# Optimization experiments

Measured on AMD Instinct MI355X. Metric: run time of the kernel, lower is better.

The kernel has to match this reference:

```python
import jax, jax.numpy as jnp
import numpy as np

N_NODES = 100000


def gcn_conv(x, edge_index, W, b, n_nodes):
    """PyG GCNConv: out = D^-1/2 (A + I) D^-1/2 (x @ W^T) + b."""
    src, dst = edge_index[0], edge_index[1]
    loop = jnp.arange(n_nodes, dtype=src.dtype)
    src = jnp.concatenate([src, loop])  # [E + N]
    dst = jnp.concatenate([dst, loop])
    # degree of each node as aggregation target (includes self loop)
    deg = jax.ops.segment_sum(jnp.ones_like(src, dtype=x.dtype), dst,
                              num_segments=n_nodes)
    deg_inv_sqrt = jnp.where(deg > 0, jax.lax.rsqrt(deg), 0.0)
    norm = deg_inv_sqrt[src] * deg_inv_sqrt[dst]  # [E + N]
    h = x @ W.T  # [N, out_dim]  (transform BEFORE propagate, as in PyG)
    msg = h[src] * norm[:, None]  # gather + scale  [E + N, out_dim]
    out = jax.ops.segment_sum(msg, dst, num_segments=n_nodes)  # scatter-add
    return out + b


def setup_inputs() -> dict:
    key = jax.random.key(0)
    k_x, k_e, k_w1, k_b1, k_w2, k_b2 = jax.random.split(key, 6)
    in_dim, hidden = 128, 16
    n_edges = 3200000
    x = jax.random.normal(k_x, (N_NODES, in_dim), dtype=jnp.float32)
    edge_index = jax.random.randint(k_e, (2, n_edges), 0, N_NODES,
                                    dtype=jnp.int64)
    # Glorot-ish init for the linear weights (PyG Linear stores [out, in])
    W1 = jax.random.normal(k_w1, (hidden, in_dim), dtype=jnp.float32) / np.sqrt(in_dim)
    b1 = jnp.zeros((hidden,), dtype=jnp.float32)
    W2 = jax.random.normal(k_w2, (1, hidden), dtype=jnp.float32) / np.sqrt(hidden)
    b2 = jnp.zeros((1,), dtype=jnp.float32)
    return {"x": x, "edge_index": edge_index,
            "W1": W1, "b1": b1, "W2": W2, "b2": b2}


def reference(x, edge_index, W1, b1, W2, b2):
    n = x.shape[0]
    h = jax.nn.relu(gcn_conv(x, edge_index, W1, b1, n))  # [N, hidden]
    out = gcn_conv(h, edge_index, W2, b2, n)  # [N, 1]
    return out.squeeze(-1)  # [N]
```

## Files before the change

### kernel.cpp

```cpp
#include <hip/hip_runtime.h>

#define IN_DIM 128
#define HID 16
#define BSHIFT 8
#define BMASK  255
#define BCAP   9216
#define MID    4608
#define PCH    8192
#define FTHR   512
#define EPT    (PCH / FTHR)
#define TSCALE 4096.0f
#define ZSCALE 262144.0f

__global__ void init_kernel(const unsigned int* ei, int* flag, int* gcur) {
    int tid = blockIdx.x * blockDim.x + threadIdx.x;
    if (tid < 4096) gcur[tid] = 0;
    if (tid == 0) {
        int zeros = 0;
        for (int j = 0; j < 8; ++j)
            if (ei[2 * j + 1] == 0u) zeros++;
        *flag = (zeros >= 7) ? 1 : 0;
    }
}

__device__ __forceinline__ int edge_at(const void* ei, long long idx, int is64) {
    if (is64) return (int)((const long long*)ei)[idx];
    return ((const int*)ei)[idx];
}

__global__ __launch_bounds__(FTHR) void fat_kernel(const void* ei, long long E,
        int* gcur, unsigned int* __restrict__ binned, int NB, const int* flag,
        const float* __restrict__ x, const float* __restrict__ W1,
        short* __restrict__ ts16, int N, int pblk) {
    __shared__ float smem[4 * 128 * 17];
    int tid = threadIdx.x;
    if ((int)blockIdx.x < pblk) {
        int* cnt = (int*)smem;
        int* wbase = cnt + 1024;
        for (int i = tid; i < NB; i += FTHR) cnt[i] = 0;
        __syncthreads();
        const int is64 = *flag;
        const long long e0 = (long long)blockIdx.x * PCH;

        int sA[EPT], dA[EPT];
        if (e0 + PCH <= E) {
            if (is64) {
                const long long* p = (const long long*)ei;
#pragma unroll
                for (int j = 0; j < EPT; ++j) sA[j] = (int)p[e0 + j * FTHR + tid];
#pragma unroll
                for (int j = 0; j < EPT; ++j) dA[j] = (int)p[E + e0 + j * FTHR + tid];
            } else {
                const int* p = (const int*)ei;
#pragma unroll
                for (int j = 0; j < EPT; ++j) sA[j] = p[e0 + j * FTHR + tid];
#pragma unroll
                for (int j = 0; j < EPT; ++j) dA[j] = p[E + e0 + j * FTHR + tid];
            }
        } else {
#pragma unroll
            for (int j = 0; j < EPT; ++j) {
                long long e = e0 + j * FTHR + tid;
                bool ok = e < E;
                sA[j] = ok ? edge_at(ei, e, is64) : 0;
                dA[j] = ok ? edge_at(ei, E + e, is64) : -(BMASK + 1);
            }
        }

        unsigned int v[EPT];
        unsigned int br[EPT];
#pragma unroll
        for (int j = 0; j < EPT; ++j) {
            int b = dA[j] >> BSHIFT;
            bool ok = dA[j] >= 0;
            int r = ok ? atomicAdd(&cnt[b], 1) : 0;
            v[j]  = ((unsigned int)sA[j] << BSHIFT) | (unsigned int)(dA[j] & BMASK);
            br[j] = ok ? (((unsigned int)b << 16) | (unsigned int)r) : 0xFFFFFFFFu;
        }
        __syncthreads();
        const int q = (int)(blockIdx.x & 3);
        int* gc = gcur + q * 1024;
        for (int i = tid; i < NB; i += FTHR) {
            int c = cnt[i];
            wbase[i] = c ? atomicAdd(&gc[i], c) : 0;
        }
        __syncthreads();
        const int regBase = (q >> 1) * MID;
        const bool down = (q & 1);
#pragma unroll
        for (int j = 0; j < EPT; ++j) {
            if (br[j] != 0xFFFFFFFFu) {
                int b = (int)(br[j] >> 16);
                int r = (int)(br[j] & 0xFFFFu);
                int w = wbase[b] + r;
                if (w < MID) {
                    int pos = regBase + (down ? (MID - 1 - w) : w);
                    binned[(size_t)b * BCAP + pos] = v[j];
                }
            }
        }
    } else {
        const int nb = (int)blockIdx.x - pblk;
        const int lane = tid & 63;
        const int kq = __builtin_amdgcn_readfirstlane(tid >> 7);
        const int half = (tid >> 6) & 1;
        const int nl = half * 64 + lane;
        const int node = nb * 128 + nl;

        float acc[HID];
#pragma unroll
        for (int o = 0; o < HID; ++o) acc[o] = 0.f;
        if (node < N) {
            const float* xp = &x[(size_t)node * IN_DIM + kq * 32];
            float4 xv[8];
#pragma unroll
            for (int j = 0; j < 8; ++j) xv[j] = ((const float4*)xp)[j];
            const float* wp = &W1[kq * 32];
#pragma unroll
            for (int kk = 0; kk < 32; ++kk) {
                float xs = ((const float*)xv)[kk];
#pragma unroll
                for (int o = 0; o < HID; ++o)
                    acc[o] = fmaf(xs, wp[(size_t)o * IN_DIM + kk], acc[o]);
            }
        }
#pragma unroll
        for (int o = 0; o < HID; ++o)
            smem[((size_t)kq * 128 + nl) * 17 + o] = acc[o];
        __syncthreads();

        const int nl2 = tid >> 2;
        const int og = (tid & 3) * 4;
        const int node2 = nb * 128 + nl2;
        if (node2 < N) {
            float s0 = 0.f, s1 = 0.f, s2 = 0.f, s3 = 0.f;
#pragma unroll
            for (int w2 = 0; w2 < 4; ++w2) {
                const float* rp = &smem[((size_t)w2 * 128 + nl2) * 17 + og];
                s0 += rp[0]; s1 += rp[1]; s2 += rp[2]; s3 += rp[3];
            }
            int i0 = (int)rintf(fminf(fmaxf(TSCALE * s0, -32767.f), 32767.f));
            int i1 = (int)rintf(fminf(fmaxf(TSCALE * s1, -32767.f), 32767.f));
            int i2 = (int)rintf(fminf(fmaxf(TSCALE * s2, -32767.f), 32767.f));
            int i3 = (int)rintf(fminf(fmaxf(TSCALE * s3, -32767.f), 32767.f));
            uint2 pk;
            pk.x = ((unsigned int)i0 & 0xFFFFu) | ((unsigned int)i1 << 16);
            pk.y = ((unsigned int)i2 & 0xFFFFu) | ((unsigned int)i3 << 16);
            ((uint2*)ts16)[(size_t)node2 * 4 + (tid & 3)] = pk;
        }
    }
}

__device__ __forceinline__ void bucket_ranges(const int* gcur, int b,
        int& r0hi, int& r1lo, int& r1hi, int& r2lo) {
    int cA = gcur[b];            if (cA > MID) cA = MID;
    int cB = gcur[1024 + b];     if (cB > MID - cA) cB = MID - cA;
    int cC = gcur[2048 + b];     if (cC > MID) cC = MID;
    int cD = gcur[3072 + b];     if (cD > MID - cC) cD = MID - cC;
    r0hi = cA;
    r1lo = MID - cB;
    r1hi = MID + cC;
    r2lo = BCAP - cD;
}

__global__ __launch_bounds__(1024) void degdis_kernel(
        const unsigned int* __restrict__ binned, const int* __restrict__ gcur,
        float* __restrict__ dis, short* __restrict__ ts16, int N) {
    __shared__ int cnt[256];
    __shared__ float disl[256];
    int b = blockIdx.x, tid = threadIdx.x;
    int base = b * BCAP;
    int r0hi, r1lo, r1hi, r2lo;
    bucket_ranges(gcur, b, r0hi, r1lo, r1hi, r2lo);
    if (tid < 256) cnt[tid] = 0;
    __syncthreads();
    for (int e = tid; e < r0hi; e += 1024)
        atomicAdd(&cnt[binned[(size_t)base + e] & BMASK], 1);
    for (int e = r1lo + tid; e < r1hi; e += 1024)
        atomicAdd(&cnt[binned[(size_t)base + e] & BMASK], 1);
    for (int e = r2lo + tid; e < BCAP; e += 1024)
        atomicAdd(&cnt[binned[(size_t)base + e] & BMASK], 1);
    __syncthreads();
    if (tid < 256) {
        float dv = rsqrtf((float)(cnt[tid] + 1));
        disl[tid] = dv;
        int node = (b << BSHIFT) + tid;
        if (node < N) dis[node] = dv;
    }
    __syncthreads();
    {
        int nl = tid >> 2, part = tid & 3;
        int node = (b << BSHIFT) + nl;
        if (node < N) {
            uint2 v = ((uint2*)ts16)[(size_t)node * 4 + part];
            float dv = disl[nl];
            int a0 = (int)(short)(v.x & 0xFFFF);
            int a1 = (int)v.x >> 16;
            int a2 = (int)(short)(v.y & 0xFFFF);
            int a3 = (int)v.y >> 16;
            int r0 = (int)rintf((float)a0 * dv);
            int r1 = (int)rintf((float)a1 * dv);
            int r2 = (int)rintf((float)a2 * dv);
            int r3 = (int)rintf((float)a3 * dv);
            uint2 o;
            o.x = ((unsigned int)r0 & 0xFFFFu) | ((unsigned int)r1 << 16);
            o.y = ((unsigned int)r2 & 0xFFFFu) | ((unsigned int)r3 << 16);
            ((uint2*)ts16)[(size_t)node * 4 + part] = o;
        }
    }
}

__global__ __launch_bounds__(1024) void agg1_kernel(
        const unsigned int* __restrict__ binned, const int* __restrict__ gcur,
        const short* __restrict__ ts16, const float* __restrict__ dis,
        const float* __restrict__ b1, const float* __restrict__ W2,
        float* __restrict__ zs, int N) {
    __shared__ int acc[256 * 17];
    int b = blockIdx.x, tid = threadIdx.x;
    for (int i = tid; i < 256 * 17; i += 1024) acc[i] = 0;
    __syncthreads();
    int base = b * BCAP;
    int r0hi, r1lo, r1hi, r2lo;
    bucket_ranges(gcur, b, r0hi, r1lo, r1hi, r2lo);

#define AGG1_EDGE(IDX)                                                        \
    {                                                                         \
        unsigned int v = binned[(size_t)base + (IDX)];                        \
        int src = (int)(v >> BSHIFT);                                         \
        int row = (int)(v & BMASK) * 17;                                      \
        const int4* tp = (const int4*)(ts16 + (size_t)src * 16);              \
        int4 a = tp[0], c = tp[1];                                            \
        atomicAdd(&acc[row + 0],  (int)(short)(a.x & 0xFFFF));                \
        atomicAdd(&acc[row + 1],  a.x >> 16);                                 \
        atomicAdd(&acc[row + 2],  (int)(short)(a.y & 0xFFFF));                \
        atomicAdd(&acc[row + 3],  a.y >> 16);                                 \
        atomicAdd(&acc[row + 4],  (int)(short)(a.z & 0xFFFF));                \
        atomicAdd(&acc[row + 5],  a.z >> 16);                                 \
        atomicAdd(&acc[row + 6],  (int)(short)(a.w & 0xFFFF));                \
        atomicAdd(&acc[row + 7],  a.w >> 16);                                 \
        atomicAdd(&acc[row + 8],  (int)(short)(c.x & 0xFFFF));                \
        atomicAdd(&acc[row + 9],  c.x >> 16);                                 \
        atomicAdd(&acc[row + 10], (int)(short)(c.y & 0xFFFF));                \
        atomicAdd(&acc[row + 11], c.y >> 16);                                 \
        atomicAdd(&acc[row + 12], (int)(short)(c.z & 0xFFFF));                \
        atomicAdd(&acc[row + 13], c.z >> 16);                                 \
        atomicAdd(&acc[row + 14], (int)(short)(c.w & 0xFFFF));                \
        atomicAdd(&acc[row + 15], c.w >> 16);                                 \
    }

    for (int e = tid; e < r0hi; e += 1024) AGG1_EDGE(e)
    for (int e = r1lo + tid; e < r1hi; e += 1024) AGG1_EDGE(e)
    for (int e = r2lo + tid; e < BCAP; e += 1024) AGG1_EDGE(e)
#undef AGG1_EDGE
    __syncthreads();
    if (tid < 256) {
        int node = (b << BSHIFT) + tid;
        if (node < N) {
            float di = dis[node];
            const int4* tp = (const int4*)(ts16 + (size_t)node * 16);
            int4 a = tp[0], c = tp[1];
            int self[16] = {
                (int)(short)(a.x & 0xFFFF), a.x >> 16,
                (int)(short)(a.y & 0xFFFF), a.y >> 16,
                (int)(short)(a.z & 0xFFFF), a.z >> 16,
                (int)(short)(a.w & 0xFFFF), a.w >> 16,
                (int)(short)(c.x & 0xFFFF), c.x >> 16,
                (int)(short)(c.y & 0xFFFF), c.y >> 16,
                (int)(short)(c.z & 0xFFFF), c.z >> 16,
                (int)(short)(c.w & 0xFFFF), c.w >> 16 };
            float z = 0.f;
#pragma unroll
            for (int j = 0; j < 16; ++j) {
                float s = (float)(acc[tid * 17 + j] + self[j]) * (1.0f / TSCALE);
                float h = fmaxf(fmaf(di, s, b1[j]), 0.f);
                z = fmaf(h, W2[j], z);
            }
            zs[node] = di * z;
        }
    }
}

__global__ __launch_bounds__(1024) void agg2_kernel(
        const unsigned int* __restrict__ binned, const int* __restrict__ gcur,
        const float* __restrict__ zs, const float* __restrict__ dis,
        const float* __restrict__ b2, float* __restrict__ out, int N) {
    __shared__ int acc2[256];
    int b = blockIdx.x, tid = threadIdx.x;
    if (tid < 256) acc2[tid] = 0;
    __syncthreads();
    int base = b * BCAP;
    int r0hi, r1lo, r1hi, r2lo;
    bucket_ranges(gcur, b, r0hi, r1lo, r1hi, r2lo);
    for (int e = tid; e < r0hi; e += 1024) {
        unsigned int v = binned[(size_t)base + e];
        atomicAdd(&acc2[v & BMASK], (int)rintf(zs[v >> BSHIFT] * ZSCALE));
    }
    for (int e = r1lo + tid; e < r1hi; e += 1024) {
        unsigned int v = binned[(size_t)base + e];
        atomicAdd(&acc2[v & BMASK], (int)rintf(zs[v >> BSHIFT] * ZSCALE));
    }
    for (int e = r2lo + tid; e < BCAP; e += 1024) {
        unsigned int v = binned[(size_t)base + e];
        atomicAdd(&acc2[v & BMASK], (int)rintf(zs[v >> BSHIFT] * ZSCALE));
    }
    __syncthreads();
    if (tid < 256) {
        int node = (b << BSHIFT) + tid;
        if (node < N) {
            float s = (float)acc2[tid] * (1.0f / ZSCALE) + zs[node];
            out[node] = fmaf(dis[node], s, b2[0]);
        }
    }
}

extern "C" void kernel_launch(void* const* d_in, const int* in_sizes, int n_in,
                              void* d_out, int out_size, void* d_ws, size_t ws_size,
                              hipStream_t stream) {
    const float* x  = (const float*)d_in[0];
    const void*  ei = d_in[1];
    const float* W1 = (const float*)d_in[2];
    const float* b1 = (const float*)d_in[3];
    const float* W2 = (const float*)d_in[4];
    const float* b2 = (const float*)d_in[5];
    float* out = (float*)d_out;

    const int N = in_sizes[0] / IN_DIM;
    const long long E = in_sizes[1] / 2;
    const int NB = (N + BMASK) >> BSHIFT;

    char* w = (char*)d_ws;
    unsigned int* binned = (unsigned int*)w;  w += (size_t)NB * BCAP * sizeof(unsigned int);
    short* ts16   = (short*)w;  w += (size_t)N * HID * sizeof(short);
    float* zs     = (float*)w;  w += (size_t)N * sizeof(float);
    float* dis    = (float*)w;  w += (size_t)N * sizeof(float);
    int*   gcur   = (int*)w;    w += 4096 * sizeof(int);
    int*   flag   = (int*)w;

    init_kernel<<<16, 256, 0, stream>>>((const unsigned int*)ei, flag, gcur);

    int pblk = (int)((E + PCH - 1) / PCH);
    int gblk = (N + 127) / 128;
    fat_kernel<<<pblk + gblk, FTHR, 0, stream>>>(
        ei, E, gcur, binned, NB, flag, x, W1, ts16, N, pblk);

    degdis_kernel<<<NB, 1024, 0, stream>>>(binned, gcur, dis, ts16, N);

    agg1_kernel<<<NB, 1024, 0, stream>>>(binned, gcur, ts16, dis, b1, W2, zs, N);

    agg2_kernel<<<NB, 1024, 0, stream>>>(binned, gcur, zs, dis, b2, out, N);
}
```

Baseline: 92.62 us.

## Stage binned edges in LDS by bucket for coalesced global scatter

The partition blocks now run a block-wide prefix scan over the bucket counts, place edges in an LDS staging buffer sorted by bucket, and then write them out contiguously per bucket using a binary search to find each element's bucket. This turns the random scattered global stores into mostly contiguous runs. The chunk size is halved so the staging buffer fits in shared memory, which doubles the number of partition blocks and global atomics. It also adds a 9-step scan with barriers and a per-element binary search. cnt/wbase are shrunk to 512 entries, which assumes NB ≤ 512.

```diff
diff --git a/kernel.cpp b/kernel.cpp
--- a/kernel.cpp
+++ b/kernel.cpp
@@ -6,7 +6,7 @@
 #define BMASK  255
 #define BCAP   9216
 #define MID    4608
-#define PCH    8192
+#define PCH    4096
 #define FTHR   512
 #define EPT    (PCH / FTHR)
 #define TSCALE 4096.0f
@@ -32,11 +32,13 @@
         int* gcur, unsigned int* __restrict__ binned, int NB, const int* flag,
         const float* __restrict__ x, const float* __restrict__ W1,
         short* __restrict__ ts16, int N, int pblk) {
-    __shared__ float smem[4 * 128 * 17];
+    __shared__ int smem[4 * 128 * 17];
     int tid = threadIdx.x;
     if ((int)blockIdx.x < pblk) {
-        int* cnt = (int*)smem;
-        int* wbase = cnt + 1024;
+        int* cnt   = smem;
+        int* wbase = smem + 512;
+        int* incl  = smem + 1024;
+        unsigned int* stage = (unsigned int*)(smem + 1536);
         for (int i = tid; i < NB; i += FTHR) cnt[i] = 0;
         __syncthreads();
         const int is64 = *flag;
@@ -84,22 +86,44 @@
             int c = cnt[i];
             wbase[i] = c ? atomicAdd(&gc[i], c) : 0;
         }
-        __syncthreads();
-        const int regBase = (q >> 1) * MID;
-        const bool down = (q & 1);
+        int c0 = (tid < NB) ? cnt[tid] : 0;
+        incl[tid] = c0;
+        __syncthreads();
+        for (int off = 1; off < 512; off <<= 1) {
+            int t_ = (tid >= off) ? incl[tid - off] : 0;
+            __syncthreads();
+            incl[tid] += t_;
+            __syncthreads();
+        }
 #pragma unroll
         for (int j = 0; j < EPT; ++j) {
             if (br[j] != 0xFFFFFFFFu) {
                 int b = (int)(br[j] >> 16);
                 int r = (int)(br[j] & 0xFFFFu);
-                int w = wbase[b] + r;
-                if (w < MID) {
-                    int pos = regBase + (down ? (MID - 1 - w) : w);
-                    binned[(size_t)b * BCAP + pos] = v[j];
-                }
+                int pos = incl[b] - cnt[b] + r;
+                stage[pos] = v[j];
+            }
+        }
+        __syncthreads();
+        const int total = incl[511];
+        const int regBase = (q >> 1) * MID;
+        const bool down = (q & 1);
+        for (int i = tid; i < total; i += FTHR) {
+            int lo = 0, hi = NB;
+            while (lo < hi) {
+                int mid = (lo + hi) >> 1;
+                if (incl[mid] <= i) lo = mid + 1; else hi = mid;
+            }
+            int b = lo;
+            int local = i - (incl[b] - cnt[b]);
+            int w = wbase[b] + local;
+            if (w < MID) {
+                int pos = regBase + (down ? (MID - 1 - w) : w);
+                binned[(size_t)b * BCAP + pos] = stage[i];
             }
         }
     } else {
+        float* red = (float*)smem;
         const int nb = (int)blockIdx.x - pblk;
         const int lane = tid & 63;
         const int kq = __builtin_amdgcn_readfirstlane(tid >> 7);
@@ -126,7 +150,7 @@
         }
 #pragma unroll
         for (int o = 0; o < HID; ++o)
-            smem[((size_t)kq * 128 + nl) * 17 + o] = acc[o];
+            red[((size_t)kq * 128 + nl) * 17 + o] = acc[o];
         __syncthreads();
 
         const int nl2 = tid >> 2;
@@ -136,7 +160,7 @@
             float s0 = 0.f, s1 = 0.f, s2 = 0.f, s3 = 0.f;
 #pragma unroll
             for (int w2 = 0; w2 < 4; ++w2) {
-                const float* rp = &smem[((size_t)w2 * 128 + nl2) * 17 + og];
+                const float* rp = &red[((size_t)w2 * 128 + nl2) * 17 + og];
                 s0 += rp[0]; s1 += rp[1]; s2 += rp[2]; s3 += rp[3];
             }
             int i0 = (int)rintf(fminf(fmaxf(TSCALE * s0, -32767.f), 32767.f));
```

Result: faster. 87.39 us (-5.6%).
